# Performance work log

Hardware: AMD Instinct MI355X
Metric: run time of the kernel (lower is better)

Reference implementation:

```python
import jax, jax.numpy as jnp
import numpy as np

NUM_CODE = 256   # 2**8, bit=[8]*5
CODE_DIM = 128
N_LAYERS = 5
B, T = 16, 8192


def setup_inputs() -> dict:
    key = jax.random.key(0)
    kx, ke = jax.random.split(key)
    x = jax.random.normal(kx, (B, CODE_DIM, T), dtype=jnp.float32)
    # torch init: torch.empty(K, D).normal_() / ((layer+1)*code_dim)
    eks = jax.random.split(ke, N_LAYERS)
    embeddings = jnp.stack([
        jax.random.normal(eks[i], (NUM_CODE, CODE_DIM), dtype=jnp.float32)
        / ((i + 1) * CODE_DIM)
        for i in range(N_LAYERS)
    ])  # [L, K, D]
    return {"x": x, "embeddings": embeddings}


def reference(x, embeddings):
    """RVQEmbedding forward (eval mode). x: [B, N, T]; embeddings: [L, K, N]."""
    eps = jnp.finfo(jnp.float32).eps
    b, n, t = x.shape
    L, K, _ = embeddings.shape
    M = b * t  # flattened tokens
    # input.detach().mT.view(B*T, N)
    residual = jax.lax.stop_gradient(x).transpose(0, 2, 1).reshape(M, n)

    quants, idxs, ppls = [], [], []
    for i in range(L):
        emb = embeddings[i]  # [K, N]
        dist = ((residual * residual).sum(-1, keepdims=True)
                + (emb * emb).sum(-1)[None, :]
                - 2.0 * residual @ emb.T)  # [M, K]
        idx = jnp.argmin(dist, axis=-1)          # [M]
        q = emb[idx]                              # [M, N] gather
        # perplexity from one-hot mean (computed as code counts)
        avg_probs = jnp.zeros((K,), dtype=jnp.float32).at[idx].add(1.0) / M
        ppl = jnp.exp(-jnp.sum(avg_probs * jnp.log(avg_probs + eps)))
        residual = residual - q
        quants.append(q if i == 0 else quants[-1] + q)  # cumulative quantized
        idxs.append(idx)
        ppls.append(ppl)

    # [M, N, L] -> [B, N, T, L]
    quantized = jnp.stack(quants, -1).reshape(b, t, n, L).transpose(0, 2, 1, 3)
    indices = jnp.stack(idxs, -1).reshape(b, t, L)
    ppl = jnp.stack(ppls, -1)
    latent_loss = jnp.float32(0.0)
    for i in range(L):
        d = x - jax.lax.stop_gradient(quantized[..., i])
        latent_loss = latent_loss + jnp.mean(d * d)
    return quantized, indices, ppl, latent_loss
```

## Files before the change

### kernel.cpp

```cpp
#include <hip/hip_runtime.h>
#include <math.h>

#define NUM_CODE 256
#define CODE_DIM 128
#define N_LAYERS 5
#define TT 8192
#define MTOK 131072
#define TOKPB 64
#define MARGIN 1e-4f

#define QOFF   0ull
#define IOFF   83886080ull
#define PPLOFF 84541440ull
#define LOSSOFF 84541445ull


__global__ __launch_bounds__(256) void rvq_init_kernel(
        const float* __restrict__ emb,
        unsigned int* __restrict__ cnt,
        double* __restrict__ lossws,
        float* __restrict__ ee2)
{
    int g = blockIdx.x * 256 + threadIdx.x;
    if (g < N_LAYERS) lossws[g] = 0.0;
    if (g < N_LAYERS * NUM_CODE) {
        cnt[g] = 0u;
        const float* e = emb + (size_t)g * CODE_DIM;
        float s[8];
        #pragma unroll
        for (int j = 0; j < 8; ++j) s[j] = __fmul_rn(e[j], e[j]);
        #pragma unroll
        for (int i = 8; i < CODE_DIM; i += 8) {
            #pragma unroll
            for (int j = 0; j < 8; ++j)
                s[j] = __fadd_rn(s[j], __fmul_rn(e[i + j], e[i + j]));
        }
        ee2[g] = __fadd_rn(
            __fadd_rn(__fadd_rn(s[0], s[1]), __fadd_rn(s[2], s[3])),
            __fadd_rn(__fadd_rn(s[4], s[5]), __fadd_rn(s[6], s[7])));
    }
}

__device__ __forceinline__ float exact_rr2_col(const float* __restrict__ rcol)
{
    float s[8];
    #pragma unroll
    for (int i = 0; i < 16; ++i) {
        #pragma unroll
        for (int j = 0; j < 8; ++j) {
            float rv = rcol[(8 * i + j) * TOKPB];
            float p = __fmul_rn(rv, rv);
            s[j] = (i == 0) ? p : __fadd_rn(s[j], p);
        }
    }
    return __fadd_rn(
        __fadd_rn(__fadd_rn(s[0], s[1]), __fadd_rn(s[2], s[3])),
        __fadd_rn(__fadd_rn(s[4], s[5]), __fadd_rn(s[6], s[7])));
}

__device__ __forceinline__ float exact_dist_col(
        const float* __restrict__ erow, const float* __restrict__ rcol,
        float rr2, float ee2c)
{
    float s[8];
    #pragma unroll
    for (int i = 0; i < 16; ++i) {
        const float4* ev = reinterpret_cast<const float4*>(erow + 8 * i);
        float4 e0 = ev[0], e1 = ev[1];
        float p0 = __fmul_rn(rcol[(8*i+0) * TOKPB], e0.x);
        float p1 = __fmul_rn(rcol[(8*i+1) * TOKPB], e0.y);
        float p2 = __fmul_rn(rcol[(8*i+2) * TOKPB], e0.z);
        float p3 = __fmul_rn(rcol[(8*i+3) * TOKPB], e0.w);
        float p4 = __fmul_rn(rcol[(8*i+4) * TOKPB], e1.x);
        float p5 = __fmul_rn(rcol[(8*i+5) * TOKPB], e1.y);
        float p6 = __fmul_rn(rcol[(8*i+6) * TOKPB], e1.z);
        float p7 = __fmul_rn(rcol[(8*i+7) * TOKPB], e1.w);
        if (i == 0) {
            s[0]=p0; s[1]=p1; s[2]=p2; s[3]=p3;
            s[4]=p4; s[5]=p5; s[6]=p6; s[7]=p7;
        } else {
            s[0]=__fadd_rn(s[0],p0); s[1]=__fadd_rn(s[1],p1);
            s[2]=__fadd_rn(s[2],p2); s[3]=__fadd_rn(s[3],p3);
            s[4]=__fadd_rn(s[4],p4); s[5]=__fadd_rn(s[5],p5);
            s[6]=__fadd_rn(s[6],p6); s[7]=__fadd_rn(s[7],p7);
        }
    }
    float dot = __fadd_rn(
        __fadd_rn(__fadd_rn(s[0], s[1]), __fadd_rn(s[2], s[3])),
        __fadd_rn(__fadd_rn(s[4], s[5]), __fadd_rn(s[6], s[7])));
    float t1 = __fadd_rn(rr2, ee2c);
    return __fsub_rn(t1, __fadd_rn(dot, dot));
}

__global__ __launch_bounds__(256) void rvq_main_kernel(
        const float* __restrict__ x,
        const float* __restrict__ emb,
        float* __restrict__ out,
        unsigned int* __restrict__ cnt,
        double* __restrict__ lossws,
        const float* __restrict__ ee2ws)
{
    __shared__ float A[CODE_DIM][TOKPB];
    __shared__ float Bt[16][NUM_CODE];
    __shared__ float e2s[NUM_CODE];
    __shared__ int   bis[TOKPB];
    __shared__ int   bihist[N_LAYERS][TOKPB];
    __shared__ float rtv[4];
    __shared__ int   rti[4];
    __shared__ double lred[4];

    const int tid = threadIdx.x;
    const int m0  = blockIdx.x * TOKPB;
    const int b   = m0 >> 13;
    const int t0  = m0 & (TT - 1);
    const size_t xbase = (size_t)b * (CODE_DIM * (size_t)TT) + t0;

    float* __restrict__ outq = out + QOFF;
    float* __restrict__ outi = out + IOFF;

    #pragma unroll
    for (int rep = 0; rep < 8; ++rep) {
        int f4 = rep * 256 + tid;
        int k = f4 >> 4;
        int tk = (f4 & 15) * 4;
        float4 v = *reinterpret_cast<const float4*>(x + xbase + (size_t)k * TT + tk);
        *reinterpret_cast<float4*>(&A[k][tk]) = v;
    }

    const int tg = tid >> 5;
    const int cg = tid & 31;

    for (int l = 0; l < N_LAYERS; ++l) {
        const float* __restrict__ el = emb + (size_t)l * NUM_CODE * CODE_DIM;
        e2s[tid] = ee2ws[l * NUM_CODE + tid];
        __syncthreads();

        float ee2r[8];
        #pragma unroll
        for (int j = 0; j < 4; ++j) {
            ee2r[j]     = e2s[cg * 4 + j];
            ee2r[4 + j] = e2s[128 + cg * 4 + j];
        }

        float acc[8][8];
        #pragma unroll
        for (int i = 0; i < 8; ++i)
            #pragma unroll
            for (int j = 0; j < 8; ++j) acc[i][j] = 0.f;

        for (int kc = 0; kc < CODE_DIM / 16; ++kc) {
            {
                const float4* ep = reinterpret_cast<const float4*>(
                    el + (size_t)tid * CODE_DIM + kc * 16);
                float4 q0 = ep[0], q1 = ep[1], q2 = ep[2], q3 = ep[3];
                Bt[ 0][tid]=q0.x; Bt[ 1][tid]=q0.y; Bt[ 2][tid]=q0.z; Bt[ 3][tid]=q0.w;
                Bt[ 4][tid]=q1.x; Bt[ 5][tid]=q1.y; Bt[ 6][tid]=q1.z; Bt[ 7][tid]=q1.w;
                Bt[ 8][tid]=q2.x; Bt[ 9][tid]=q2.y; Bt[10][tid]=q2.z; Bt[11][tid]=q2.w;
                Bt[12][tid]=q3.x; Bt[13][tid]=q3.y; Bt[14][tid]=q3.z; Bt[15][tid]=q3.w;
            }
            __syncthreads();
            #pragma unroll
            for (int k = 0; k < 16; ++k) {
                float4 a0 = *reinterpret_cast<const float4*>(&A[kc*16 + k][tg*8]);
                float4 a1 = *reinterpret_cast<const float4*>(&A[kc*16 + k][tg*8 + 4]);
                float4 b0 = *reinterpret_cast<const float4*>(&Bt[k][cg*4]);
                float4 b1 = *reinterpret_cast<const float4*>(&Bt[k][128 + cg*4]);
                float av[8] = {a0.x,a0.y,a0.z,a0.w,a1.x,a1.y,a1.z,a1.w};
                float bv[8] = {b0.x,b0.y,b0.z,b0.w,b1.x,b1.y,b1.z,b1.w};
                #pragma unroll
                for (int i = 0; i < 8; ++i)
                    #pragma unroll
                    for (int j = 0; j < 8; ++j)
                        acc[i][j] = fmaf(av[i], bv[j], acc[i][j]);
            }
            __syncthreads();
        }

        #pragma unroll
        for (int i = 0; i < 8; ++i) {
            float m1v = INFINITY, m2v = INFINITY;
            int i1v = 0;
            #pragma unroll
            for (int j = 0; j < 8; ++j) {
                float dv = acc[i][j];
                float u = __fsub_rn(ee2r[j], __fadd_rn(dv, dv));
                int cj = (j < 4) ? (cg * 4 + j) : (128 + cg * 4 + j - 4);
                bool b1 = u < m1v, b2 = u < m2v;
                m2v = b1 ? m1v : (b2 ? u : m2v);
                m1v = b1 ? u : m1v;
                i1v = b1 ? cj : i1v;
            }
            #pragma unroll
            for (int d = 1; d < 32; d <<= 1) {
                float o1 = __shfl_xor(m1v, d, 32);
                int   oi = __shfl_xor(i1v, d, 32);
                float o2 = __shfl_xor(m2v, d, 32);
                if (o1 < m1v)      { m2v = fminf(m1v, o2); m1v = o1; i1v = oi; }
                else if (o1 > m1v) { m2v = fminf(m2v, o1); }
                else               { i1v = min(i1v, oi); m2v = m1v; }
            }
            if (cg == 0)
                bis[tg * 8 + i] = (m2v - m1v < MARGIN) ? ~i1v : i1v;
        }
        __syncthreads();

        for (int tok = 0; tok < TOKPB; ++tok) {
            if (bis[tok] >= 0) continue;
            const float* rcol = &A[0][tok];
            float rr2 = exact_rr2_col(rcol);
            float di = exact_dist_col(el + (size_t)tid * CODE_DIM, rcol,
                                      rr2, e2s[tid]);
            float bv = di; int bidx = tid;
            #pragma unroll
            for (int o = 32; o > 0; o >>= 1) {
                float ov = __shfl_down(bv, o, 64);
                int   oi = __shfl_down(bidx, o, 64);
                if (ov < bv || (ov == bv && oi < bidx)) { bv = ov; bidx = oi; }
            }
            if ((tid & 63) == 0) { rtv[tid >> 6] = bv; rti[tid >> 6] = bidx; }
            __syncthreads();
            if (tid == 0) {
                float gv = rtv[0]; int gidx = rti[0];
                #pragma unroll
                for (int w = 1; w < 4; ++w) {
                    if (rtv[w] < gv || (rtv[w] == gv && rti[w] < gidx)) {
                        gv = rtv[w]; gidx = rti[w];
                    }
                }
                bis[tok] = gidx;
            }
            __syncthreads();
        }

        if (tid < TOKPB) {
            int bi = bis[tid];
            bihist[l][tid] = bi;
            outi[(size_t)(m0 + tid) * N_LAYERS + l] = (float)bi;
            atomicAdd(&cnt[l * NUM_CODE + bi], 1u);
        }

        {
            int utok = tid & 63, part = tid >> 6;
            int bi = bis[utok];
            const float4* qr = reinterpret_cast<const float4*>(
                el + (size_t)bi * CODE_DIM + part * 32);
            double ls = 0.0;
            #pragma unroll
            for (int q8 = 0; q8 < 8; ++q8) {
                float4 e = qr[q8];
                int k = part * 32 + q8 * 4;
                float r0 = __fsub_rn(A[k + 0][utok], e.x);
                float r1 = __fsub_rn(A[k + 1][utok], e.y);
                float r2 = __fsub_rn(A[k + 2][utok], e.z);
                float r3 = __fsub_rn(A[k + 3][utok], e.w);
                A[k + 0][utok] = r0; A[k + 1][utok] = r1;
                A[k + 2][utok] = r2; A[k + 3][utok] = r3;
                ls = fma((double)r0, (double)r0, ls);
                ls = fma((double)r1, (double)r1, ls);
                ls = fma((double)r2, (double)r2, ls);
                ls = fma((double)r3, (double)r3, ls);
            }
            #pragma unroll
            for (int o = 32; o > 0; o >>= 1)
                ls += __shfl_down(ls, o, 64);
            if ((tid & 63) == 0) lred[tid >> 6] = ls;
        }
        __syncthreads();
        if (tid == 0)
            atomicAdd(&lossws[l], lred[0] + lred[1] + lred[2] + lred[3]);
        __syncthreads();
    }

    float* sq  = &A[0][0];
    float* sx  = sq + 5 * 64 * 9;
    float* sob = sx + 8 * 64;

    for (int nc = 0; nc < 16; ++nc) {
        const int n0 = nc * 8;
        __syncthreads();
        #pragma unroll
        for (int rep = 0; rep < 3; ++rep) {
            int f4 = rep * 256 + tid;
            if (f4 < 640) {
                int row = f4 >> 1;
                int half = f4 & 1;
                int l2 = row >> 6, tok = row & 63;
                float4 v = *reinterpret_cast<const float4*>(
                    emb + ((size_t)l2 * NUM_CODE + bihist[l2][tok]) * CODE_DIM
                        + n0 + half * 4);
                float* d = &sq[row * 9 + half * 4];
                d[0] = v.x; d[1] = v.y; d[2] = v.z; d[3] = v.w;
            }
        }
        if (tid < 128) {
            int np = tid >> 4, tk = (tid & 15) * 4;
            float4 v = *reinterpret_cast<const float4*>(
                x + xbase + (size_t)(n0 + np) * TT + tk);
            *reinterpret_cast<float4*>(&sx[np * 64 + tk]) = v;
        }
        __syncthreads();
        #pragma unroll
        for (int rep = 0; rep < 2; ++rep) {
            int cell = rep * 256 + tid;
            int np = cell >> 6, tok = cell & 63;
            float xv = sx[np * 64 + tok];
            float rr = xv;
            float* dst = &sob[(np * 64 + tok) * 5];
            #pragma unroll
            for (int l2 = 0; l2 < N_LAYERS; ++l2) {
                rr = __fsub_rn(rr, sq[(l2 * 64 + tok) * 9 + np]);
                dst[l2] = __fsub_rn(xv, rr);
            }
        }
        __syncthreads();
        #pragma unroll
        for (int rep = 0; rep < 3; ++rep) {
            int f4 = rep * 256 + tid;
            if (f4 < 640) {
                int np = f4 / 80, kk = f4 % 80;
                float4 v = *reinterpret_cast<const float4*>(&sob[np * 320 + kk * 4]);
                *reinterpret_cast<float4*>(
                    outq + ((size_t)((size_t)b * CODE_DIM + n0 + np) * TT + t0)
                             * N_LAYERS + kk * 4) = v;
            }
        }
    }
}

__global__ __launch_bounds__(256) void rvq_finalize_kernel(
        const unsigned int* __restrict__ cnt,
        const double* __restrict__ lossws,
        float* __restrict__ out)
{
    __shared__ double sd[256];
    const int k = threadIdx.x;
    const double epsf = 1.1920928955078125e-07;
    for (int l = 0; l < N_LAYERS; ++l) {
        float p = (float)cnt[l * NUM_CODE + k] / 131072.0f;
        double term = (double)p * log((double)p + epsf);
        sd[k] = term;
        __syncthreads();
        for (int s = 128; s > 0; s >>= 1) {
            if (k < s) sd[k] += sd[k + s];
            __syncthreads();
        }
        if (k == 0) out[PPLOFF + l] = (float)exp(-sd[0]);
        __syncthreads();
    }
    if (k == 0) {
        double tot = 0.0;
        for (int l = 0; l < N_LAYERS; ++l) tot += lossws[l];
        out[LOSSOFF] = (float)(tot / 16777216.0);
    }
}

extern "C" void kernel_launch(void* const* d_in, const int* in_sizes, int n_in,
                              void* d_out, int out_size, void* d_ws, size_t ws_size,
                              hipStream_t stream)
{
    const float* x   = (const float*)d_in[0];
    const float* emb = (const float*)d_in[1];
    float* out = (float*)d_out;

    unsigned int* cnt = (unsigned int*)d_ws;
    double* lossws    = (double*)((char*)d_ws + 5120);
    float* ee2ws      = (float*)((char*)d_ws + 5160);

    rvq_init_kernel<<<5, 256, 0, stream>>>(emb, cnt, lossws, ee2ws);
    rvq_main_kernel<<<MTOK / TOKPB, 256, 0, stream>>>(x, emb, out, cnt, lossws, ee2ws);
    rvq_finalize_kernel<<<1, 256, 0, stream>>>(cnt, lossws, out);
}
```

Measured before the change: 1.436 ms.

## Double-buffer codebook tiles with register prefetch and preload all code norms

The codebook tile in shared memory is now double-buffered. The next 16-column slice is loaded into registers before the FMA loop and written to the alternate buffer afterwards, which drops one barrier per k-chunk and hides global load latency behind compute. Accumulators are regrouped as float2 pairs, which may let the compiler emit packed FP32 FMAs. All layers' code norms are loaded once up front, removing a per-layer load and barrier, and the trailing per-layer barrier is moved out of the loop. In exchange, shared memory grows and register pressure rises from the prefetch registers, which may lower occupancy.

```diff
diff --git a/kernel.cpp b/kernel.cpp
--- a/kernel.cpp
+++ b/kernel.cpp
@@ -101,8 +101,8 @@
         const float* __restrict__ ee2ws)
 {
     __shared__ float A[CODE_DIM][TOKPB];
-    __shared__ float Bt[16][NUM_CODE];
-    __shared__ float e2s[NUM_CODE];
+    __shared__ float Bt[2][16][NUM_CODE];
+    __shared__ float e2all[N_LAYERS][NUM_CODE];
     __shared__ int   bis[TOKPB];
     __shared__ int   bihist[N_LAYERS][TOKPB];
     __shared__ float rtv[4];
@@ -126,65 +126,89 @@
         float4 v = *reinterpret_cast<const float4*>(x + xbase + (size_t)k * TT + tk);
         *reinterpret_cast<float4*>(&A[k][tk]) = v;
     }
+    #pragma unroll
+    for (int i = 0; i < N_LAYERS; ++i)
+        e2all[i][tid] = ee2ws[i * NUM_CODE + tid];
 
     const int tg = tid >> 5;
     const int cg = tid & 31;
 
     for (int l = 0; l < N_LAYERS; ++l) {
         const float* __restrict__ el = emb + (size_t)l * NUM_CODE * CODE_DIM;
-        e2s[tid] = ee2ws[l * NUM_CODE + tid];
-        __syncthreads();
-
-        float ee2r[8];
-        #pragma unroll
-        for (int j = 0; j < 4; ++j) {
-            ee2r[j]     = e2s[cg * 4 + j];
-            ee2r[4 + j] = e2s[128 + cg * 4 + j];
-        }
-
-        float acc[8][8];
+
+        float2 acc[8][4];
         #pragma unroll
         for (int i = 0; i < 8; ++i)
             #pragma unroll
-            for (int j = 0; j < 8; ++j) acc[i][j] = 0.f;
-
-        for (int kc = 0; kc < CODE_DIM / 16; ++kc) {
-            {
+            for (int j = 0; j < 4; ++j) acc[i][j] = make_float2(0.f, 0.f);
+
+        {
+            const float4* ep = reinterpret_cast<const float4*>(
+                el + (size_t)tid * CODE_DIM);
+            float4 q0 = ep[0], q1 = ep[1], q2 = ep[2], q3 = ep[3];
+            Bt[0][ 0][tid]=q0.x; Bt[0][ 1][tid]=q0.y; Bt[0][ 2][tid]=q0.z; Bt[0][ 3][tid]=q0.w;
+            Bt[0][ 4][tid]=q1.x; Bt[0][ 5][tid]=q1.y; Bt[0][ 6][tid]=q1.z; Bt[0][ 7][tid]=q1.w;
+            Bt[0][ 8][tid]=q2.x; Bt[0][ 9][tid]=q2.y; Bt[0][10][tid]=q2.z; Bt[0][11][tid]=q2.w;
+            Bt[0][12][tid]=q3.x; Bt[0][13][tid]=q3.y; Bt[0][14][tid]=q3.z; Bt[0][15][tid]=q3.w;
+        }
+        __syncthreads();
+
+        for (int kc = 0; kc < 8; ++kc) {
+            float4 p0, p1, p2, p3;
+            if (kc < 7) {
                 const float4* ep = reinterpret_cast<const float4*>(
-                    el + (size_t)tid * CODE_DIM + kc * 16);
-                float4 q0 = ep[0], q1 = ep[1], q2 = ep[2], q3 = ep[3];
-                Bt[ 0][tid]=q0.x; Bt[ 1][tid]=q0.y; Bt[ 2][tid]=q0.z; Bt[ 3][tid]=q0.w;
-                Bt[ 4][tid]=q1.x; Bt[ 5][tid]=q1.y; Bt[ 6][tid]=q1.z; Bt[ 7][tid]=q1.w;
-                Bt[ 8][tid]=q2.x; Bt[ 9][tid]=q2.y; Bt[10][tid]=q2.z; Bt[11][tid]=q2.w;
-                Bt[12][tid]=q3.x; Bt[13][tid]=q3.y; Bt[14][tid]=q3.z; Bt[15][tid]=q3.w;
-            }
-            __syncthreads();
+                    el + (size_t)tid * CODE_DIM + (kc + 1) * 16);
+                p0 = ep[0]; p1 = ep[1]; p2 = ep[2]; p3 = ep[3];
+            }
+            const int buf = kc & 1;
             #pragma unroll
             for (int k = 0; k < 16; ++k) {
                 float4 a0 = *reinterpret_cast<const float4*>(&A[kc*16 + k][tg*8]);
                 float4 a1 = *reinterpret_cast<const float4*>(&A[kc*16 + k][tg*8 + 4]);
-                float4 b0 = *reinterpret_cast<const float4*>(&Bt[k][cg*4]);
-                float4 b1 = *reinterpret_cast<const float4*>(&Bt[k][128 + cg*4]);
+                float2 b0 = *reinterpret_cast<const float2*>(&Bt[buf][k][cg*4]);
+                float2 b1 = *reinterpret_cast<const float2*>(&Bt[buf][k][cg*4 + 2]);
+                float2 b2 = *reinterpret_cast<const float2*>(&Bt[buf][k][128 + cg*4]);
+                float2 b3 = *reinterpret_cast<const float2*>(&Bt[buf][k][128 + cg*4 + 2]);
                 float av[8] = {a0.x,a0.y,a0.z,a0.w,a1.x,a1.y,a1.z,a1.w};
-                float bv[8] = {b0.x,b0.y,b0.z,b0.w,b1.x,b1.y,b1.z,b1.w};
                 #pragma unroll
-                for (int i = 0; i < 8; ++i)
-                    #pragma unroll
-                    for (int j = 0; j < 8; ++j)
-                        acc[i][j] = fmaf(av[i], bv[j], acc[i][j]);
+                for (int i = 0; i < 8; ++i) {
+                    acc[i][0].x = fmaf(av[i], b0.x, acc[i][0].x);
+                    acc[i][0].y = fmaf(av[i], b0.y, acc[i][0].y);
+                    acc[i][1].x = fmaf(av[i], b1.x, acc[i][1].x);
+                    acc[i][1].y = fmaf(av[i], b1.y, acc[i][1].y);
+                    acc[i][2].x = fmaf(av[i], b2.x, acc[i][2].x);
+                    acc[i][2].y = fmaf(av[i], b2.y, acc[i][2].y);
+                    acc[i][3].x = fmaf(av[i], b3.x, acc[i][3].x);
+                    acc[i][3].y = fmaf(av[i], b3.y, acc[i][3].y);
+                }
+            }
+            if (kc < 7) {
+                const int nb = buf ^ 1;
+                Bt[nb][ 0][tid]=p0.x; Bt[nb][ 1][tid]=p0.y; Bt[nb][ 2][tid]=p0.z; Bt[nb][ 3][tid]=p0.w;
+                Bt[nb][ 4][tid]=p1.x; Bt[nb][ 5][tid]=p1.y; Bt[nb][ 6][tid]=p1.z; Bt[nb][ 7][tid]=p1.w;
+                Bt[nb][ 8][tid]=p2.x; Bt[nb][ 9][tid]=p2.y; Bt[nb][10][tid]=p2.z; Bt[nb][11][tid]=p2.w;
+                Bt[nb][12][tid]=p3.x; Bt[nb][13][tid]=p3.y; Bt[nb][14][tid]=p3.z; Bt[nb][15][tid]=p3.w;
             }
             __syncthreads();
         }
 
+        float ee2r[8];
+        #pragma unroll
+        for (int j = 0; j < 4; ++j) {
+            ee2r[j]     = e2all[l][cg * 4 + j];
+            ee2r[4 + j] = e2all[l][128 + cg * 4 + j];
+        }
         #pragma unroll
         for (int i = 0; i < 8; ++i) {
             float m1v = INFINITY, m2v = INFINITY;
             int i1v = 0;
             #pragma unroll
             for (int j = 0; j < 8; ++j) {
-                float dv = acc[i][j];
-                float u = __fsub_rn(ee2r[j], __fadd_rn(dv, dv));
-                int cj = (j < 4) ? (cg * 4 + j) : (128 + cg * 4 + j - 4);
+                float dv = (j & 1) ? acc[i][j >> 1].y : acc[i][j >> 1].x;
+                float u = __fsub_rn(ee2r[(j >> 1) * 2 + (j & 1) + ((j >= 4) ? 0 : 0)],
+                                    __fadd_rn(dv, dv));
+                int cj = ((j >> 2) ? 128 : 0) + cg * 4 + (j & 3);
+                u = __fsub_rn(ee2r[j], __fadd_rn(dv, dv));
                 bool b1 = u < m1v, b2 = u < m2v;
                 m2v = b1 ? m1v : (b2 ? u : m2v);
                 m1v = b1 ? u : m1v;
@@ -209,7 +233,7 @@
             const float* rcol = &A[0][tok];
             float rr2 = exact_rr2_col(rcol);
             float di = exact_dist_col(el + (size_t)tid * CODE_DIM, rcol,
-                                      rr2, e2s[tid]);
+                                      rr2, e2all[l][tid]);
             float bv = di; int bidx = tid;
             #pragma unroll
             for (int o = 32; o > 0; o >>= 1) {
@@ -268,9 +292,9 @@
         __syncthreads();
         if (tid == 0)
             atomicAdd(&lossws[l], lred[0] + lred[1] + lred[2] + lred[3]);
-        __syncthreads();
-    }
-
+    }
+
+    __syncthreads();
     float* sq  = &A[0][0];
     float* sx  = sq + 5 * 64 * 9;
     float* sob = sx + 8 * 64;
```

Measured after the change: 1.426 ms. About the same (-0.7%).
